# Kernel tuning notes

Hardware: AMD Instinct MI355X
Metric: run time of the kernel (lower is better)

## Reference

```python
import jax, jax.numpy as jnp
import numpy as np

B, N, P = 8, 4096, 1024
P4 = P // 4
EPS = 1e-5


def _ln(x, g, b):
    mu = jnp.mean(x, axis=-1, keepdims=True)
    var = jnp.var(x, axis=-1, keepdims=True)
    return (x - mu) * jax.lax.rsqrt(var + EPS) * g + b


def setup_inputs() -> dict:
    key = jax.random.key(0)
    ks = jax.random.split(key, 16)
    s = lambda fan: 1.0 / np.sqrt(fan)
    return {
        "xyz": jax.random.normal(ks[0], (B, N, 3), jnp.float32),
        "x": jax.random.normal(ks[1], (B, N, P), jnp.float32),
        "ln1_g": jnp.ones((P,), jnp.float32),
        "ln1_b": jnp.zeros((P,), jnp.float32),
        "ln2_g": jnp.ones((P,), jnp.float32),
        "ln2_b": jnp.zeros((P,), jnp.float32),
        "qk_w": jax.random.normal(ks[2], (P4, P), jnp.float32) * s(P),   # shared q/k 1x1 conv, no bias
        "v_w": jax.random.normal(ks[3], (P, P), jnp.float32) * s(P),
        "v_b": jax.random.normal(ks[4], (P,), jnp.float32) * s(P),
        "t1_w": jax.random.normal(ks[5], (P, P4), jnp.float32) * s(P4),  # trans_conv
        "t1_b": jax.random.normal(ks[6], (P,), jnp.float32) * s(P4),
        "t2_w": jax.random.normal(ks[7], (P, P4), jnp.float32) * s(P4),  # trans_conv1
        "t2_b": jax.random.normal(ks[8], (P,), jnp.float32) * s(P4),
        "m1_w": jax.random.normal(ks[9], (P, P), jnp.float32) * s(P),
        "m1_b": jax.random.normal(ks[10], (P,), jnp.float32) * s(P),
        "m2_w": jax.random.normal(ks[11], (P, P), jnp.float32) * s(P),
        "m2_b": jax.random.normal(ks[12], (P,), jnp.float32) * s(P),
    }


def reference(xyz, x, ln1_g, ln1_b, ln2_g, ln2_b, qk_w, v_w, v_b,
              t1_w, t1_b, t2_w, t2_b, m1_w, m1_b, m2_w, m2_b):
    # xyz is accepted but unused, matching the torch module. Dropout = eval identity.
    res1 = x
    h = _ln(x, ln1_g, ln1_b)                                   # [B,N,P]
    # TransformerBlock_1 (1x1 convs on h^T [B,P,N] are just matmuls over P)
    x_q = jnp.einsum('op,bnp->bon', qk_w, h)                   # [B,P4,N]
    # k shares weights with q; x_k permuted is x_q transposed
    x_v = jnp.einsum('op,bnp->bno', v_w, h) + v_b              # [B,N,P]
    energy = jnp.einsum('bqn,bkn->bqk', x_q, x_q)              # [B,P4,P4]
    att = jnp.einsum('op,bpk->bok', t1_w, energy) + t1_b[:, None]   # [B,P,P4]
    att = jax.nn.gelu(att, approximate=False)
    att = jnp.einsum('op,bkp->bok', t2_w, att) + t2_b[:, None]      # [B,P,P]
    att = jax.nn.softmax(att, axis=-1)
    t_out = jnp.einsum('bnp,bpq->bnq', x_v, att)               # [B,N,P]
    x1 = t_out + res1
    h2 = _ln(x1, ln2_g, ln2_b)
    m = jax.nn.gelu(h2 @ m1_w.T + m1_b, approximate=False)
    m = m @ m2_w.T + m2_b
    return x1 + m
```

## Files before the change

kernel.cpp:

```cpp
#include <hip/hip_runtime.h>


typedef __attribute__((ext_vector_type(4))) float f32x4;
typedef __attribute__((ext_vector_type(8))) _Float16 h16x8;
typedef __attribute__((ext_vector_type(8))) unsigned short u16x8;
typedef __attribute__((ext_vector_type(4))) unsigned short u16x4;

__device__ __forceinline__ unsigned short f2h(float f) {
  _Float16 h = (_Float16)f;
  return __builtin_bit_cast(unsigned short, h);
}
__device__ __forceinline__ float h2f(unsigned short u) {
  return (float)__builtin_bit_cast(_Float16, u);
}
__device__ __forceinline__ unsigned split16(float f) {
  _Float16 h = (_Float16)f;
  _Float16 l = (_Float16)(f - (float)h);
  return (unsigned)__builtin_bit_cast(unsigned short, h) |
         ((unsigned)__builtin_bit_cast(unsigned short, l) << 16);
}
__device__ __forceinline__ float gelu_f(float x) {
  return 0.5f * x * (1.0f + erff(x * 0.70710678118654752f));
}
__device__ __forceinline__ void gload16(const void* g, void* l) {
  __builtin_amdgcn_global_load_lds(
      (const __attribute__((address_space(1))) unsigned int*)g,
      (__attribute__((address_space(3))) unsigned int*)l, 16, 0, 0);
}
#define FENCE() asm volatile("" ::: "memory")

__device__ __forceinline__ void xcd_swz(int& bx, int& by, int gx, int gy) {
  const int nwg = gx * gy;
  if ((nwg & 7) == 0 && nwg >= 16) {
    const int flat = bx + gx * by;
    const int chunk = nwg >> 3;
    const int nf = (flat & 7) * chunk + (flat >> 3);
    bx = nf % gx;
    by = nf / gx;
  }
}

__global__ __launch_bounds__(256)
void ln_kernel(const float* __restrict__ x, const float* __restrict__ g,
               const float* __restrict__ b, unsigned short* __restrict__ hi,
               unsigned short* __restrict__ lo, unsigned short* __restrict__ xh) {
  __shared__ float red[16];
  const size_t base = (size_t)blockIdx.x * 1024;
  const int t = threadIdx.x;
  f32x4 v = *(const f32x4*)&x[base + t * 4];
  float s = v[0] + v[1] + v[2] + v[3];
  float q = v[0] * v[0] + v[1] * v[1] + v[2] * v[2] + v[3] * v[3];
#pragma unroll
  for (int o = 32; o > 0; o >>= 1) { s += __shfl_down(s, o); q += __shfl_down(q, o); }
  const int w = t >> 6;
  if ((t & 63) == 0) { red[w] = s; red[8 + w] = q; }
  __syncthreads();
  s = (red[0] + red[1]) + (red[2] + red[3]);
  q = (red[8] + red[9]) + (red[10] + red[11]);
  const float mu = s * (1.0f / 1024.0f);
  const float var = q * (1.0f / 1024.0f) - mu * mu;
  const float is = rsqrtf(var + 1e-5f);
  f32x4 gg = *(const f32x4*)&g[t * 4];
  f32x4 bb = *(const f32x4*)&b[t * 4];
  u16x4 oh, ol, ox;
#pragma unroll
  for (int j = 0; j < 4; j++) {
    float y = (v[j] - mu) * is * gg[j] + bb[j];
    unsigned p = split16(y);
    oh[j] = (unsigned short)(p & 0xffffu);
    ol[j] = (unsigned short)(p >> 16);
    ox[j] = f2h(v[j]);
  }
  *(u16x4*)&hi[base + t * 4] = oh;
  if (lo) *(u16x4*)&lo[base + t * 4] = ol;
  if (xh) *(u16x4*)&xh[base + t * 4] = ox;
}

__global__ __launch_bounds__(256)
void ln16_kernel(const unsigned short* __restrict__ x16, const float* __restrict__ g,
                 const float* __restrict__ b, unsigned short* __restrict__ hi) {
  __shared__ float red[16];
  const size_t base = (size_t)blockIdx.x * 1024;
  const int t = threadIdx.x;
  u16x4 raw = *(const u16x4*)&x16[base + t * 4];
  float v[4];
#pragma unroll
  for (int j = 0; j < 4; j++) v[j] = h2f(raw[j]);
  float s = v[0] + v[1] + v[2] + v[3];
  float q = v[0] * v[0] + v[1] * v[1] + v[2] * v[2] + v[3] * v[3];
#pragma unroll
  for (int o = 32; o > 0; o >>= 1) { s += __shfl_down(s, o); q += __shfl_down(q, o); }
  const int w = t >> 6;
  if ((t & 63) == 0) { red[w] = s; red[8 + w] = q; }
  __syncthreads();
  s = (red[0] + red[1]) + (red[2] + red[3]);
  q = (red[8] + red[9]) + (red[10] + red[11]);
  const float mu = s * (1.0f / 1024.0f);
  const float var = q * (1.0f / 1024.0f) - mu * mu;
  const float is = rsqrtf(var + 1e-5f);
  f32x4 gg = *(const f32x4*)&g[t * 4];
  f32x4 bb = *(const f32x4*)&b[t * 4];
  u16x4 oh;
#pragma unroll
  for (int j = 0; j < 4; j++) oh[j] = f2h((v[j] - mu) * is * gg[j] + bb[j]);
  *(u16x4*)&hi[base + t * 4] = oh;
}

__global__ __launch_bounds__(256)
void cvt_kernel(const float* __restrict__ in, unsigned short* __restrict__ hi,
                unsigned short* __restrict__ lo, int n4) {
  int i = blockIdx.x * 256 + threadIdx.x;
  if (i < n4) {
    f32x4 v = *(const f32x4*)&in[(size_t)i * 4];
    u16x4 oh, ol;
#pragma unroll
    for (int j = 0; j < 4; j++) {
      unsigned p = split16(v[j]);
      oh[j] = (unsigned short)(p & 0xffffu);
      ol[j] = (unsigned short)(p >> 16);
    }
    *(u16x4*)&hi[(size_t)i * 4] = oh;
    if (lo) *(u16x4*)&lo[(size_t)i * 4] = ol;
  }
}

__global__ __launch_bounds__(256)
void vwt_kernel(const float* __restrict__ vw, unsigned short* __restrict__ wvt) {
  __shared__ float T[64][65];
  const int bx = blockIdx.x, by = blockIdx.y;
  const int t = threadIdx.x;
  const int lr = t >> 6, lc = t & 63;
#pragma unroll
  for (int i = 0; i < 16; ++i) {
    const int row = i * 4 + lr;
    T[row][lc] = vw[(size_t)(by * 64 + row) * 1024 + bx * 64 + lc];
  }
  __syncthreads();
#pragma unroll
  for (int i = 0; i < 16; ++i) {
    const int row = i * 4 + lr;
    wvt[(size_t)(bx * 64 + row) * 1024 + by * 64 + lc] = f2h(T[lc][row]);
  }
}

__global__ __launch_bounds__(256)
void beff_kernel(const unsigned short* __restrict__ attT, const float* __restrict__ vb,
                 float* __restrict__ beff) {
  const int b = blockIdx.y;
  const int q = blockIdx.x * 4 + (threadIdx.x >> 6);
  const int l = threadIdx.x & 63;
  const unsigned short* row = attT + ((size_t)b * 1024 + q) * 1024;
  float s = 0.0f;
#pragma unroll
  for (int i = 0; i < 2; ++i) {
    u16x8 v = *(const u16x8*)&row[(i * 64 + l) * 8];
    f32x4 vb0 = *(const f32x4*)&vb[(i * 64 + l) * 8];
    f32x4 vb1 = *(const f32x4*)&vb[(i * 64 + l) * 8 + 4];
#pragma unroll
    for (int j = 0; j < 4; j++) s += h2f(v[j]) * vb0[j];
#pragma unroll
    for (int j = 0; j < 4; j++) s += h2f(v[j + 4]) * vb1[j];
  }
#pragma unroll
  for (int o = 32; o > 0; o >>= 1) s += __shfl_down(s, o);
  if (l == 0) beff[b * 1024 + q] = s;
}

template <int EPI>
__global__ __launch_bounds__(256)
void gemm_v(const unsigned short* __restrict__ Ain, const unsigned short* __restrict__ Bin,
            void* __restrict__ Cout, const float* __restrict__ bias,
            const unsigned short* __restrict__ res16In,
            int K, int lda, int ldb, int ldc,
            long long sA, long long sB, long long sC, long long sBias, long long sRes) {
  __shared__ short As[2][4096];
  __shared__ short Bs[2][4096];
  const int z = blockIdx.z;
  const unsigned short* A = Ain + (size_t)z * sA;
  const unsigned short* B = Bin + (size_t)z * sB;
  int bx = blockIdx.x, by = blockIdx.y;
  xcd_swz(bx, by, gridDim.x, gridDim.y);
  const int mBase = by * 128, nBase = bx * 128;
  const int t = threadIdx.x, w = t >> 6, l = t & 63;
  const int r16 = l & 15, kq = l >> 4;
  const int wr = (w >> 1) * 64, wc = (w & 1) * 64;
  f32x4 acc[4][4] = {};

  auto stage = [&](int buf, int k0) {
#pragma unroll
    for (int i = 0; i < 2; ++i) {
      const int c = i * 256 + t;
      const int row = c >> 2, cc = c & 3;
      const int gc = cc ^ ((row >> 1) & 3);
      short* la = &As[buf][(i * 256 + w * 64) * 8];
      short* lb = &Bs[buf][(i * 256 + w * 64) * 8];
      gload16(&A[(size_t)(mBase + row) * lda + k0 + gc * 8], la);
      gload16(&B[(size_t)(nBase + row) * ldb + k0 + gc * 8], lb);
    }
  };

  const int nt = K >> 5;
  stage(0, 0);
  if (nt > 1) stage(1, 32);
  for (int ts = 0; ts < nt; ++ts) {
    const int cur = ts & 1;
    if (ts + 1 < nt) { asm volatile("s_waitcnt vmcnt(4)" ::: "memory"); }
    else             { asm volatile("s_waitcnt vmcnt(0)" ::: "memory"); }
    __builtin_amdgcn_s_barrier();
    FENCE();
    h16x8 aF[4], bF[4];
#pragma unroll
    for (int mi = 0; mi < 4; mi++) {
      const int r = wr + mi * 16 + r16;
      aF[mi] = *(const h16x8*)&As[cur][r * 32 + (kq ^ ((r >> 1) & 3)) * 8];
    }
#pragma unroll
    for (int ni = 0; ni < 4; ni++) {
      const int r = wc + ni * 16 + r16;
      bF[ni] = *(const h16x8*)&Bs[cur][r * 32 + (kq ^ ((r >> 1) & 3)) * 8];
    }
    __builtin_amdgcn_s_setprio(1);
#pragma unroll
    for (int mi = 0; mi < 4; mi++)
#pragma unroll
      for (int ni = 0; ni < 4; ni++)
        acc[mi][ni] = __builtin_amdgcn_mfma_f32_16x16x32_f16(aF[mi], bF[ni], acc[mi][ni], 0, 0, 0);
    __builtin_amdgcn_s_setprio(0);
    FENCE();
    __builtin_amdgcn_s_barrier();
    FENCE();
    if (ts + 2 < nt) stage(cur, (ts + 2) * 32);
  }
  FENCE();

  unsigned short* C16 = (unsigned short*)Cout + (size_t)z * sC;
  float* C32 = (float*)Cout + (size_t)z * sC;
  const float* bp = (EPI == 1 || EPI == 3 || EPI == 8) ? bias + (size_t)z * sBias : nullptr;
  const unsigned short* rp = (EPI == 3 || EPI == 8) ? res16In + (size_t)z * sRes : nullptr;

  if constexpr (EPI == 1 || EPI == 4 || EPI == 8) {
    short* ep = ((w & 2) ? &Bs[0][0] : &As[0][0]) + (w & 1) * 4096;
#pragma unroll
    for (int mi = 0; mi < 4; mi++) {
#pragma unroll
      for (int ni = 0; ni < 4; ni++) {
        const int cl = nBase + wc + ni * 16 + r16;
        const float bcol = bp ? bp[cl] : 0.0f;
#pragma unroll
        for (int r = 0; r < 4; r++) {
          float v = acc[mi][ni][r] + bcol;
          if (EPI == 1) v = gelu_f(v);
          ep[(mi * 16 + kq * 4 + r) * 64 + ni * 16 + r16] = (short)f2h(v);
        }
      }
    }
#pragma unroll
    for (int j = 0; j < 8; j++) {
      const int f = j * 512 + l * 8;
      const int row = f >> 6, col = f & 63;
      u16x8 v8 = *(const u16x8*)&ep[f];
      const size_t gi = (size_t)(mBase + wr + row) * ldc + nBase + wc + col;
      if (EPI == 8) {
        u16x8 r8 = *(const u16x8*)&rp[gi];
#pragma unroll
        for (int q = 0; q < 8; q++) v8[q] = f2h(h2f(v8[q]) + h2f(r8[q]));
      }
      *(u16x8*)&C16[gi] = v8;
    }
  } else {
#pragma unroll
    for (int mi = 0; mi < 4; mi++) {
#pragma unroll
      for (int ni = 0; ni < 4; ni++) {
        const int cl = nBase + wc + ni * 16 + r16;
        const float bcol = bp[cl];
#pragma unroll
        for (int r = 0; r < 4; r++) {
          const int rw = mBase + wr + mi * 16 + kq * 4 + r;
          const size_t idx = (size_t)rw * ldc + cl;
          C32[idx] = acc[mi][ni][r] + bcol + h2f(rp[idx]);
        }
      }
    }
  }
}

template <int EPI>
__global__ __launch_bounds__(256)
void gemm_s(const unsigned short* __restrict__ Ahi, const unsigned short* __restrict__ Alo,
            const unsigned short* __restrict__ Bhi, const unsigned short* __restrict__ Blo,
            void* __restrict__ Cout, unsigned short* __restrict__ Cout2,
            const float* __restrict__ bias,
            int K, int lda, int ldb, int ldc,
            long long sA, long long sB, long long sC, int splitK) {
  __shared__ short As[2][8192];
  __shared__ short Bs[2][8192];
  const int z = blockIdx.z;
  const int bi = z / splitK, sp = z % splitK;
  const int kLen = K / splitK, kStart = sp * kLen;
  const unsigned short* AH = Ahi + (size_t)bi * sA;
  const unsigned short* BH = Bhi + (size_t)bi * sB;
  const unsigned short* AL = Alo + (size_t)bi * sA;
  const unsigned short* BL = Blo + (size_t)bi * sB;
  int bx = blockIdx.x, by = blockIdx.y;
  xcd_swz(bx, by, gridDim.x, gridDim.y);
  const int mBase = by * 128, nBase = bx * 128;
  const int t = threadIdx.x, w = t >> 6, l = t & 63;
  const int r16 = l & 15, kq = l >> 4;
  const int wr = (w >> 1) * 64, wc = (w & 1) * 64;
  f32x4 acc[4][4] = {};

  auto stage = [&](int buf, int k0) {
#pragma unroll
    for (int i = 0; i < 2; ++i) {
      const int c = i * 256 + t;
      const int row = c >> 2, cc = c & 3;
      const int gc = cc ^ ((row >> 1) & 3);
      const int cbase = i * 256 + w * 64;
      const size_t ga = (size_t)(mBase + row) * lda + k0 + gc * 8;
      const size_t gb = (size_t)(nBase + row) * ldb + k0 + gc * 8;
      gload16(&AH[ga], &As[buf][cbase * 8]);
      gload16(&AL[ga], &As[buf][4096 + cbase * 8]);
      gload16(&BH[gb], &Bs[buf][cbase * 8]);
      gload16(&BL[gb], &Bs[buf][4096 + cbase * 8]);
    }
  };

  const int nsteps = kLen >> 5;
  stage(0, kStart);
  if (nsteps > 1) stage(1, kStart + 32);
  for (int ts = 0; ts < nsteps; ++ts) {
    const int cur = ts & 1;
    if (ts + 1 < nsteps) { asm volatile("s_waitcnt vmcnt(8)" ::: "memory"); }
    else                 { asm volatile("s_waitcnt vmcnt(0)" ::: "memory"); }
    __builtin_amdgcn_s_barrier();
    FENCE();
    h16x8 aH[4], bH[4], aL[4], bL[4];
#pragma unroll
    for (int mi = 0; mi < 4; mi++) {
      const int r = wr + mi * 16 + r16;
      const int off = r * 32 + (kq ^ ((r >> 1) & 3)) * 8;
      aH[mi] = *(const h16x8*)&As[cur][off];
      aL[mi] = *(const h16x8*)&As[cur][4096 + off];
    }
#pragma unroll
    for (int ni = 0; ni < 4; ni++) {
      const int r = wc + ni * 16 + r16;
      const int off = r * 32 + (kq ^ ((r >> 1) & 3)) * 8;
      bH[ni] = *(const h16x8*)&Bs[cur][off];
      bL[ni] = *(const h16x8*)&Bs[cur][4096 + off];
    }
    __builtin_amdgcn_s_setprio(1);
#pragma unroll
    for (int mi = 0; mi < 4; mi++)
#pragma unroll
      for (int ni = 0; ni < 4; ni++) {
        acc[mi][ni] = __builtin_amdgcn_mfma_f32_16x16x32_f16(aH[mi], bH[ni], acc[mi][ni], 0, 0, 0);
        acc[mi][ni] = __builtin_amdgcn_mfma_f32_16x16x32_f16(aH[mi], bL[ni], acc[mi][ni], 0, 0, 0);
        acc[mi][ni] = __builtin_amdgcn_mfma_f32_16x16x32_f16(aL[mi], bH[ni], acc[mi][ni], 0, 0, 0);
      }
    __builtin_amdgcn_s_setprio(0);
    FENCE();
    __builtin_amdgcn_s_barrier();
    FENCE();
    if (ts + 2 < nsteps) stage(cur, kStart + (ts + 2) * 32);
  }
  FENCE();

  unsigned short* C16 = (unsigned short*)Cout + (size_t)z * sC;
  unsigned short* C16b = Cout2 ? Cout2 + (size_t)z * sC : nullptr;
  float* C32 = (float*)Cout + (size_t)z * sC;

  if constexpr (EPI == 4 || EPI == 6) {
    short* ep = &As[0][0] + w * 4096;
    unsigned pk[4][4][4];
#pragma unroll
    for (int mi = 0; mi < 4; mi++)
#pragma unroll
      for (int ni = 0; ni < 4; ni++)
#pragma unroll
        for (int r = 0; r < 4; r++) {
          float v = acc[mi][ni][r];
          if (EPI == 6) { v += bias[mBase + wr + mi * 16 + kq * 4 + r]; v = gelu_f(v); }
          pk[mi][ni][r] = split16(v);
        }
#pragma unroll
    for (int mi = 0; mi < 4; mi++)
#pragma unroll
      for (int ni = 0; ni < 4; ni++)
#pragma unroll
        for (int r = 0; r < 4; r++)
          ep[(mi * 16 + kq * 4 + r) * 64 + ni * 16 + r16] =
              (short)(pk[mi][ni][r] & 0xffffu);
#pragma unroll
    for (int j = 0; j < 8; j++) {
      const int f = j * 512 + l * 8;
      const int row = f >> 6, col = f & 63;
      *(u16x8*)&C16[(size_t)(mBase + wr + row) * ldc + nBase + wc + col] =
          *(const u16x8*)&ep[f];
    }
#pragma unroll
    for (int mi = 0; mi < 4; mi++)
#pragma unroll
      for (int ni = 0; ni < 4; ni++)
#pragma unroll
        for (int r = 0; r < 4; r++)
          ep[(mi * 16 + kq * 4 + r) * 64 + ni * 16 + r16] =
              (short)(pk[mi][ni][r] >> 16);
#pragma unroll
    for (int j = 0; j < 8; j++) {
      const int f = j * 512 + l * 8;
      const int row = f >> 6, col = f & 63;
      *(u16x8*)&C16b[(size_t)(mBase + wr + row) * ldc + nBase + wc + col] =
          *(const u16x8*)&ep[f];
    }
  } else {
#pragma unroll
    for (int mi = 0; mi < 4; mi++) {
#pragma unroll
      for (int ni = 0; ni < 4; ni++) {
        const int cl = nBase + wc + ni * 16 + r16;
#pragma unroll
        for (int r = 0; r < 4; r++) {
          const int rw = mBase + wr + mi * 16 + kq * 4 + r;
          float v = acc[mi][ni][r];
          if (EPI == 7) v += bias[rw];
          C32[(size_t)rw * ldc + cl] = v;
        }
      }
    }
  }
}

__global__ __launch_bounds__(256)
void ereduce_kernel(const float* __restrict__ part, unsigned short* __restrict__ ehi,
                    unsigned short* __restrict__ elo) {
  const size_t idx = (size_t)blockIdx.x * 256 + threadIdx.x;
  const size_t b = idx >> 16, i = idx & 65535;
  const float* p = part + b * (8ull * 65536) + i;
  float s0 = (p[0] + p[65536]) + (p[2 * 65536] + p[3 * 65536]);
  float s1 = (p[4 * 65536] + p[5 * 65536]) + (p[6 * 65536] + p[7 * 65536]);
  unsigned pk = split16(s0 + s1);
  ehi[idx] = (unsigned short)(pk & 0xffffu);
  elo[idx] = (unsigned short)(pk >> 16);
}

__global__ __launch_bounds__(256)
void smax_t_kernel(const float* __restrict__ a2, unsigned short* __restrict__ attT) {
  __shared__ float S[8][1028];
  __shared__ float inv[8];
  const int t = threadIdx.x;
  const int b = blockIdx.y;
  const int o0 = blockIdx.x * 8;
  const float* src = a2 + ((size_t)b * 1024 + o0) * 1024;
#pragma unroll
  for (int i = 0; i < 8; i++)
    *(f32x4*)&S[i][t * 4] = *(const f32x4*)&src[(size_t)i * 1024 + t * 4];
  __syncthreads();
  const int w = t >> 6, l = t & 63;
  for (int rr = 0; rr < 2; rr++) {
    const int r = w * 2 + rr;
    float m = -1e30f;
#pragma unroll
    for (int i = 0; i < 16; i++) m = fmaxf(m, S[r][l + i * 64]);
#pragma unroll
    for (int o = 32; o > 0; o >>= 1) m = fmaxf(m, __shfl_xor(m, o));
    float ssum = 0.0f;
#pragma unroll
    for (int i = 0; i < 16; i++) {
      float e = expf(S[r][l + i * 64] - m);
      S[r][l + i * 64] = e;
      ssum += e;
    }
#pragma unroll
    for (int o = 32; o > 0; o >>= 1) ssum += __shfl_xor(ssum, o);
    if (l == 0) inv[r] = 1.0f / ssum;
  }
  __syncthreads();
  float iv[8];
#pragma unroll
  for (int r = 0; r < 8; r++) iv[r] = inv[r];
#pragma unroll
  for (int i = 0; i < 4; i++) {
    const int k = i * 256 + t;
    u16x8 ov;
#pragma unroll
    for (int r = 0; r < 8; r++) ov[r] = f2h(S[r][k] * iv[r]);
    *(u16x8*)&attT[((size_t)b * 1024 + k) * 1024 + o0] = ov;
  }
}

extern "C" void kernel_launch(void* const* d_in, const int* in_sizes, int n_in,
                              void* d_out, int out_size, void* d_ws, size_t ws_size,
                              hipStream_t stream) {
  (void)in_sizes; (void)n_in; (void)out_size; (void)ws_size;
  const float* x     = (const float*)d_in[1];
  const float* ln1_g = (const float*)d_in[2];
  const float* ln1_b = (const float*)d_in[3];
  const float* ln2_g = (const float*)d_in[4];
  const float* ln2_b = (const float*)d_in[5];
  const float* qk_w  = (const float*)d_in[6];
  const float* v_w   = (const float*)d_in[7];
  const float* v_b   = (const float*)d_in[8];
  const float* t1_w  = (const float*)d_in[9];
  const float* t1_b  = (const float*)d_in[10];
  const float* t2_w  = (const float*)d_in[11];
  const float* t2_b  = (const float*)d_in[12];
  const float* m1_w  = (const float*)d_in[13];
  const float* m1_b  = (const float*)d_in[14];
  const float* m2_w  = (const float*)d_in[15];
  const float* m2_b  = (const float*)d_in[16];

  char* ws = (char*)d_ws;
  unsigned short* hhi  = (unsigned short*)(ws + 0);
  unsigned short* hlo  = (unsigned short*)(ws + 67108864);
  unsigned short* Qthi = (unsigned short*)(ws + 134217728);
  unsigned short* Qtlo = (unsigned short*)(ws + 150994944);
  float*          part = (float*)(ws + 167772160);
  unsigned short* Ehi  = (unsigned short*)(ws + 184549376);
  unsigned short* Elo  = (unsigned short*)(ws + 185597952);
  unsigned short* Ghi  = (unsigned short*)(ws + 186646528);
  unsigned short* Glo  = (unsigned short*)(ws + 190840832);
  float*          a2   = (float*)(ws + 195035136);
  unsigned short* attT = (unsigned short*)(ws + 228589568);
  unsigned short* WeT  = (unsigned short*)(ws + 245366784);
  float*          beff = (float*)(ws + 262144000);
  unsigned short* xh   = (unsigned short*)(ws + 268435456);
  unsigned short* x1h  = (unsigned short*)(ws + 335544320);
  unsigned short* wqh  = (unsigned short*)(ws + 446693376);
  unsigned short* wql  = (unsigned short*)(ws + 447217664);
  unsigned short* wvt  = (unsigned short*)(ws + 447741952);
  unsigned short* wt1h = (unsigned short*)(ws + 449839104);
  unsigned short* wt1l = (unsigned short*)(ws + 450363392);
  unsigned short* wt2h = (unsigned short*)(ws + 450887680);
  unsigned short* wt2l = (unsigned short*)(ws + 451411968);
  unsigned short* wm1  = (unsigned short*)(ws + 451936256);
  unsigned short* wm2  = (unsigned short*)(ws + 454033408);
  unsigned short* h2 = hhi;
  unsigned short* gb = hlo;
  float* out = (float*)d_out;

  cvt_kernel<<<dim3(256),  dim3(256), 0, stream>>>(qk_w, wqh, wql, 65536);
  vwt_kernel<<<dim3(16, 16), dim3(256), 0, stream>>>(v_w, wvt);
  cvt_kernel<<<dim3(256),  dim3(256), 0, stream>>>(t1_w, wt1h, wt1l, 65536);
  cvt_kernel<<<dim3(256),  dim3(256), 0, stream>>>(t2_w, wt2h, wt2l, 65536);
  cvt_kernel<<<dim3(1024), dim3(256), 0, stream>>>(m1_w, wm1, nullptr, 262144);
  cvt_kernel<<<dim3(1024), dim3(256), 0, stream>>>(m2_w, wm2, nullptr, 262144);
  ln_kernel<<<dim3(32768), dim3(256), 0, stream>>>(x, ln1_g, ln1_b, hhi, hlo, xh);
  gemm_s<4><<<dim3(32, 2, 8), dim3(256), 0, stream>>>(
      wqh, wql, hhi, hlo, Qthi, Qtlo, nullptr,
      1024, 1024, 1024, 4096, 0, 4194304, 1048576, 1);
  gemm_s<5><<<dim3(2, 2, 64), dim3(256), 0, stream>>>(
      Qthi, Qtlo, Qthi, Qtlo, part, nullptr, nullptr,
      4096, 4096, 4096, 256, 1048576, 1048576, 65536, 8);
  ereduce_kernel<<<dim3(2048), dim3(256), 0, stream>>>(part, Ehi, Elo);
  gemm_s<6><<<dim3(2, 8, 8), dim3(256), 0, stream>>>(
      wt1h, wt1l, Ehi, Elo, Ghi, Glo, t1_b,
      256, 256, 256, 256, 0, 65536, 262144, 1);
  gemm_s<7><<<dim3(8, 8, 8), dim3(256), 0, stream>>>(
      wt2h, wt2l, Ghi, Glo, a2, nullptr, t2_b,
      256, 256, 256, 1024, 0, 262144, 1048576, 1);
  smax_t_kernel<<<dim3(128, 8), dim3(256), 0, stream>>>(a2, attT);
  gemm_v<4><<<dim3(8, 8, 8), dim3(256), 0, stream>>>(
      attT, wvt, WeT, nullptr, nullptr,
      1024, 1024, 1024, 1024, 1048576, 0, 1048576, 0, 0);
  beff_kernel<<<dim3(256, 8), dim3(256), 0, stream>>>(attT, v_b, beff);
  gemm_v<8><<<dim3(8, 32, 8), dim3(256), 0, stream>>>(
      hhi, WeT, x1h, beff, xh,
      1024, 1024, 1024, 1024, 4194304, 1048576, 4194304, 1024, 4194304);
  ln16_kernel<<<dim3(32768), dim3(256), 0, stream>>>(x1h, ln2_g, ln2_b, h2);
  gemm_v<1><<<dim3(8, 256, 1), dim3(256), 0, stream>>>(
      h2, wm1, gb, m1_b, nullptr, 1024, 1024, 1024, 1024, 0, 0, 0, 0, 0);
  gemm_v<3><<<dim3(8, 256, 1), dim3(256), 0, stream>>>(
      gb, wm2, out, m2_b, x1h, 1024, 1024, 1024, 1024, 0, 0, 0, 0, 0);
}
```

Measured before the change: 655.0 us.

## Fuse LN2 normalization into MLP1 GEMM load path and stage epilogues via LDS

```diff
diff --git a/kernel.cpp b/kernel.cpp
--- a/kernel.cpp
+++ b/kernel.cpp
@@ -77,8 +77,7 @@
 }
 
 __global__ __launch_bounds__(256)
-void ln16_kernel(const unsigned short* __restrict__ x16, const float* __restrict__ g,
-                 const float* __restrict__ b, unsigned short* __restrict__ hi) {
+void stats16_kernel(const unsigned short* __restrict__ x16, float* __restrict__ muis) {
   __shared__ float red[16];
   const size_t base = (size_t)blockIdx.x * 1024;
   const int t = threadIdx.x;
@@ -93,17 +92,14 @@
   const int w = t >> 6;
   if ((t & 63) == 0) { red[w] = s; red[8 + w] = q; }
   __syncthreads();
-  s = (red[0] + red[1]) + (red[2] + red[3]);
-  q = (red[8] + red[9]) + (red[10] + red[11]);
-  const float mu = s * (1.0f / 1024.0f);
-  const float var = q * (1.0f / 1024.0f) - mu * mu;
-  const float is = rsqrtf(var + 1e-5f);
-  f32x4 gg = *(const f32x4*)&g[t * 4];
-  f32x4 bb = *(const f32x4*)&b[t * 4];
-  u16x4 oh;
-#pragma unroll
-  for (int j = 0; j < 4; j++) oh[j] = f2h((v[j] - mu) * is * gg[j] + bb[j]);
-  *(u16x4*)&hi[base + t * 4] = oh;
+  if (t == 0) {
+    s = (red[0] + red[1]) + (red[2] + red[3]);
+    q = (red[8] + red[9]) + (red[10] + red[11]);
+    const float mu = s * (1.0f / 1024.0f);
+    const float var = q * (1.0f / 1024.0f) - mu * mu;
+    muis[blockIdx.x * 2] = mu;
+    muis[blockIdx.x * 2 + 1] = rsqrtf(var + 1e-5f);
+  }
 }
 
 __global__ __launch_bounds__(256)
@@ -285,7 +281,234 @@
   }
 }
 
-template <int EPI>
+__global__ __launch_bounds__(256)
+void gemm_r(const unsigned short* __restrict__ Ain, const unsigned short* __restrict__ Bin,
+            unsigned short* __restrict__ Cout, const float* __restrict__ bias,
+            const unsigned short* __restrict__ resIn,
+            int K, int lda, int ldb, int ldc,
+            long long sA, long long sB, long long sC, long long sBias, long long sRes) {
+  __shared__ short As[2][4096];
+  __shared__ short Bs[2][4096];
+  const int z = blockIdx.z;
+  const unsigned short* A = Ain + (size_t)z * sA;
+  const unsigned short* B = Bin + (size_t)z * sB;
+  int bx = blockIdx.x, by = blockIdx.y;
+  xcd_swz(bx, by, gridDim.x, gridDim.y);
+  const int mBase = by * 128, nBase = bx * 128;
+  const int t = threadIdx.x, w = t >> 6, l = t & 63;
+  const int r16 = l & 15, kq = l >> 4;
+  const int wr = (w >> 1) * 64, wc = (w & 1) * 64;
+  f32x4 acc[4][4] = {};
+
+  const int row0 = t >> 2, row1 = 64 + (t >> 2);
+  const int cc0 = t & 3;
+  const int gc0 = cc0 ^ ((row0 >> 1) & 3);
+  const int gc1 = cc0 ^ ((row1 >> 1) & 3);
+
+  u16x8 ra0, ra1, rb0, rb1;
+  auto loadreg = [&](int k0) {
+    ra0 = *(const u16x8*)&A[(size_t)(mBase + row0) * lda + k0 + gc0 * 8];
+    rb0 = *(const u16x8*)&B[(size_t)(nBase + row0) * ldb + k0 + gc0 * 8];
+    ra1 = *(const u16x8*)&A[(size_t)(mBase + row1) * lda + k0 + gc1 * 8];
+    rb1 = *(const u16x8*)&B[(size_t)(nBase + row1) * ldb + k0 + gc1 * 8];
+  };
+  auto dswrite = [&](int buf) {
+    *(u16x8*)&As[buf][t * 8] = ra0;
+    *(u16x8*)&Bs[buf][t * 8] = rb0;
+    *(u16x8*)&As[buf][(256 + t) * 8] = ra1;
+    *(u16x8*)&Bs[buf][(256 + t) * 8] = rb1;
+  };
+
+  const int nt = K >> 5;
+  loadreg(0);
+  dswrite(0);
+  if (nt > 1) loadreg(32);
+  asm volatile("s_waitcnt lgkmcnt(0)" ::: "memory");
+  __builtin_amdgcn_s_barrier();
+  FENCE();
+  for (int ts = 0; ts < nt; ++ts) {
+    const int cur = ts & 1;
+    h16x8 aF[4], bF[4];
+#pragma unroll
+    for (int mi = 0; mi < 4; mi++) {
+      const int r = wr + mi * 16 + r16;
+      aF[mi] = *(const h16x8*)&As[cur][r * 32 + (kq ^ ((r >> 1) & 3)) * 8];
+    }
+#pragma unroll
+    for (int ni = 0; ni < 4; ni++) {
+      const int r = wc + ni * 16 + r16;
+      bF[ni] = *(const h16x8*)&Bs[cur][r * 32 + (kq ^ ((r >> 1) & 3)) * 8];
+    }
+    __builtin_amdgcn_s_setprio(1);
+#pragma unroll
+    for (int mi = 0; mi < 4; mi++)
+#pragma unroll
+      for (int ni = 0; ni < 4; ni++)
+        acc[mi][ni] = __builtin_amdgcn_mfma_f32_16x16x32_f16(aF[mi], bF[ni], acc[mi][ni], 0, 0, 0);
+    __builtin_amdgcn_s_setprio(0);
+    FENCE();
+    if (ts + 1 < nt) {
+      __builtin_amdgcn_s_barrier();
+      FENCE();
+      dswrite((ts + 1) & 1);
+      if (ts + 2 < nt) loadreg((ts + 2) * 32);
+      asm volatile("s_waitcnt lgkmcnt(0)" ::: "memory");
+      FENCE();
+      __builtin_amdgcn_s_barrier();
+      FENCE();
+    }
+  }
+  FENCE();
+
+  unsigned short* C16 = Cout + (size_t)z * sC;
+  const float* bp = bias + (size_t)z * sBias;
+  const unsigned short* rp = resIn + (size_t)z * sRes;
+  short* ep = ((w & 2) ? &Bs[0][0] : &As[0][0]) + (w & 1) * 4096;
+#pragma unroll
+  for (int mi = 0; mi < 4; mi++) {
+#pragma unroll
+    for (int ni = 0; ni < 4; ni++) {
+      const int cl = nBase + wc + ni * 16 + r16;
+      const float bcol = bp[cl];
+#pragma unroll
+      for (int r = 0; r < 4; r++)
+        ep[(mi * 16 + kq * 4 + r) * 64 + ni * 16 + r16] =
+            (short)f2h(acc[mi][ni][r] + bcol);
+    }
+  }
+#pragma unroll
+  for (int j = 0; j < 8; j++) {
+    const int f = j * 512 + l * 8;
+    const int row = f >> 6, col = f & 63;
+    u16x8 v8 = *(const u16x8*)&ep[f];
+    const size_t gi = (size_t)(mBase + wr + row) * ldc + nBase + wc + col;
+    u16x8 r8 = *(const u16x8*)&rp[gi];
+#pragma unroll
+    for (int q = 0; q < 8; q++) v8[q] = f2h(h2f(v8[q]) + h2f(r8[q]));
+    *(u16x8*)&C16[gi] = v8;
+  }
+}
+
+__global__ __launch_bounds__(256)
+void gemm_m(const unsigned short* __restrict__ Ain, const unsigned short* __restrict__ Bin,
+            const float* __restrict__ muis, const float* __restrict__ lng,
+            const float* __restrict__ lnb, const float* __restrict__ bias,
+            unsigned short* __restrict__ Cout, int K, int lda, int ldb, int ldc) {
+  __shared__ short As[2][4096];
+  __shared__ short Bs[2][4096];
+  int bx = blockIdx.x, by = blockIdx.y;
+  xcd_swz(bx, by, gridDim.x, gridDim.y);
+  const int mBase = by * 128, nBase = bx * 128;
+  const int t = threadIdx.x, w = t >> 6, l = t & 63;
+  const int r16 = l & 15, kq = l >> 4;
+  const int wr = (w >> 1) * 64, wc = (w & 1) * 64;
+  f32x4 acc[4][4] = {};
+
+  const int row0 = t >> 2, row1 = 64 + (t >> 2);
+  const int cc0 = t & 3;
+  const int gc0 = cc0 ^ ((row0 >> 1) & 3);
+  const int gc1 = cc0 ^ ((row1 >> 1) & 3);
+  const float mu0 = muis[(mBase + row0) * 2], is0 = muis[(mBase + row0) * 2 + 1];
+  const float mu1 = muis[(mBase + row1) * 2], is1 = muis[(mBase + row1) * 2 + 1];
+
+  u16x8 ra0, ra1, rb0, rb1;
+  auto loadreg = [&](int k0) {
+    ra0 = *(const u16x8*)&Ain[(size_t)(mBase + row0) * lda + k0 + gc0 * 8];
+    rb0 = *(const u16x8*)&Bin[(size_t)(nBase + row0) * ldb + k0 + gc0 * 8];
+    ra1 = *(const u16x8*)&Ain[(size_t)(mBase + row1) * lda + k0 + gc1 * 8];
+    rb1 = *(const u16x8*)&Bin[(size_t)(nBase + row1) * ldb + k0 + gc1 * 8];
+  };
+  auto dswrite = [&](int buf, int k0) {
+    {
+      const int cb = k0 + gc0 * 8;
+      f32x4 g0 = *(const f32x4*)&lng[cb], g1 = *(const f32x4*)&lng[cb + 4];
+      f32x4 b0 = *(const f32x4*)&lnb[cb], b1 = *(const f32x4*)&lnb[cb + 4];
+      u16x8 o;
+#pragma unroll
+      for (int j = 0; j < 4; j++) o[j] = f2h((h2f(ra0[j]) - mu0) * is0 * g0[j] + b0[j]);
+#pragma unroll
+      for (int j = 0; j < 4; j++) o[j + 4] = f2h((h2f(ra0[j + 4]) - mu0) * is0 * g1[j] + b1[j]);
+      *(u16x8*)&As[buf][t * 8] = o;
+      *(u16x8*)&Bs[buf][t * 8] = rb0;
+    }
+    {
+      const int cb = k0 + gc1 * 8;
+      f32x4 g0 = *(const f32x4*)&lng[cb], g1 = *(const f32x4*)&lng[cb + 4];
+      f32x4 b0 = *(const f32x4*)&lnb[cb], b1 = *(const f32x4*)&lnb[cb + 4];
+      u16x8 o;
+#pragma unroll
+      for (int j = 0; j < 4; j++) o[j] = f2h((h2f(ra1[j]) - mu1) * is1 * g0[j] + b0[j]);
+#pragma unroll
+      for (int j = 0; j < 4; j++) o[j + 4] = f2h((h2f(ra1[j + 4]) - mu1) * is1 * g1[j] + b1[j]);
+      *(u16x8*)&As[buf][(256 + t) * 8] = o;
+      *(u16x8*)&Bs[buf][(256 + t) * 8] = rb1;
+    }
+  };
+
+  const int nt = K >> 5;
+  loadreg(0);
+  dswrite(0, 0);
+  if (nt > 1) loadreg(32);
+  asm volatile("s_waitcnt lgkmcnt(0)" ::: "memory");
+  __builtin_amdgcn_s_barrier();
+  FENCE();
+  for (int ts = 0; ts < nt; ++ts) {
+    const int cur = ts & 1;
+    h16x8 aF[4], bF[4];
+#pragma unroll
+    for (int mi = 0; mi < 4; mi++) {
+      const int r = wr + mi * 16 + r16;
+      aF[mi] = *(const h16x8*)&As[cur][r * 32 + (kq ^ ((r >> 1) & 3)) * 8];
+    }
+#pragma unroll
+    for (int ni = 0; ni < 4; ni++) {
+      const int r = wc + ni * 16 + r16;
+      bF[ni] = *(const h16x8*)&Bs[cur][r * 32 + (kq ^ ((r >> 1) & 3)) * 8];
+    }
+    __builtin_amdgcn_s_setprio(1);
+#pragma unroll
+    for (int mi = 0; mi < 4; mi++)
+#pragma unroll
+      for (int ni = 0; ni < 4; ni++)
+        acc[mi][ni] = __builtin_amdgcn_mfma_f32_16x16x32_f16(aF[mi], bF[ni], acc[mi][ni], 0, 0, 0);
+    __builtin_amdgcn_s_setprio(0);
+    FENCE();
+    if (ts + 1 < nt) {
+      __builtin_amdgcn_s_barrier();
+      FENCE();
+      dswrite((ts + 1) & 1, (ts + 1) * 32);
+      if (ts + 2 < nt) loadreg((ts + 2) * 32);
+      asm volatile("s_waitcnt lgkmcnt(0)" ::: "memory");
+      FENCE();
+      __builtin_amdgcn_s_barrier();
+      FENCE();
+    }
+  }
+  FENCE();
+
+  short* ep = ((w & 2) ? &Bs[0][0] : &As[0][0]) + (w & 1) * 4096;
+#pragma unroll
+  for (int mi = 0; mi < 4; mi++) {
+#pragma unroll
+    for (int ni = 0; ni < 4; ni++) {
+      const int cl = nBase + wc + ni * 16 + r16;
+      const float bcol = bias[cl];
+#pragma unroll
+      for (int r = 0; r < 4; r++)
+        ep[(mi * 16 + kq * 4 + r) * 64 + ni * 16 + r16] =
+            (short)f2h(gelu_f(acc[mi][ni][r] + bcol));
+    }
+  }
+#pragma unroll
+  for (int j = 0; j < 8; j++) {
+    const int f = j * 512 + l * 8;
+    const int row = f >> 6, col = f & 63;
+    *(u16x8*)&Cout[(size_t)(mBase + wr + row) * ldc + nBase + wc + col] =
+        *(const u16x8*)&ep[f];
+  }
+}
+
+template <int EPI, int SWAP>
 __global__ __launch_bounds__(256)
 void gemm_s(const unsigned short* __restrict__ Ahi, const unsigned short* __restrict__ Alo,
             const unsigned short* __restrict__ Bhi, const unsigned short* __restrict__ Blo,
@@ -304,7 +527,7 @@
   const unsigned short* BL = Blo + (size_t)bi * sB;
   int bx = blockIdx.x, by = blockIdx.y;
   xcd_swz(bx, by, gridDim.x, gridDim.y);
-  const int mBase = by * 128, nBase = bx * 128;
+  const int mBase = (SWAP ? bx : by) * 128, nBase = (SWAP ? by : bx) * 128;
   const int t = threadIdx.x, w = t >> 6, l = t & 63;
   const int r16 = l & 15, kq = l >> 4;
   const int wr = (w >> 1) * 64, wc = (w & 1) * 64;
@@ -525,6 +748,7 @@
   unsigned short* attT = (unsigned short*)(ws + 228589568);
   unsigned short* WeT  = (unsigned short*)(ws + 245366784);
   float*          beff = (float*)(ws + 262144000);
+  float*          muis = (float*)(ws + 262176768);
   unsigned short* xh   = (unsigned short*)(ws + 268435456);
   unsigned short* x1h  = (unsigned short*)(ws + 335544320);
   unsigned short* wqh  = (unsigned short*)(ws + 446693376);
@@ -536,7 +760,6 @@
   unsigned short* wt2l = (unsigned short*)(ws + 451411968);
   unsigned short* wm1  = (unsigned short*)(ws + 451936256);
   unsigned short* wm2  = (unsigned short*)(ws + 454033408);
-  unsigned short* h2 = hhi;
   unsigned short* gb = hlo;
   float* out = (float*)d_out;
 
@@ -547,17 +770,17 @@
   cvt_kernel<<<dim3(1024), dim3(256), 0, stream>>>(m1_w, wm1, nullptr, 262144);
   cvt_kernel<<<dim3(1024), dim3(256), 0, stream>>>(m2_w, wm2, nullptr, 262144);
   ln_kernel<<<dim3(32768), dim3(256), 0, stream>>>(x, ln1_g, ln1_b, hhi, hlo, xh);
-  gemm_s<4><<<dim3(32, 2, 8), dim3(256), 0, stream>>>(
+  gemm_s<4, 1><<<dim3(2, 32, 8), dim3(256), 0, stream>>>(
       wqh, wql, hhi, hlo, Qthi, Qtlo, nullptr,
       1024, 1024, 1024, 4096, 0, 4194304, 1048576, 1);
-  gemm_s<5><<<dim3(2, 2, 64), dim3(256), 0, stream>>>(
+  gemm_s<5, 0><<<dim3(2, 2, 64), dim3(256), 0, stream>>>(
       Qthi, Qtlo, Qthi, Qtlo, part, nullptr, nullptr,
       4096, 4096, 4096, 256, 1048576, 1048576, 65536, 8);
   ereduce_kernel<<<dim3(2048), dim3(256), 0, stream>>>(part, Ehi, Elo);
-  gemm_s<6><<<dim3(2, 8, 8), dim3(256), 0, stream>>>(
+  gemm_s<6, 0><<<dim3(2, 8, 8), dim3(256), 0, stream>>>(
       wt1h, wt1l, Ehi, Elo, Ghi, Glo, t1_b,
       256, 256, 256, 256, 0, 65536, 262144, 1);
-  gemm_s<7><<<dim3(8, 8, 8), dim3(256), 0, stream>>>(
+  gemm_s<7, 0><<<dim3(8, 8, 8), dim3(256), 0, stream>>>(
       wt2h, wt2l, Ghi, Glo, a2, nullptr, t2_b,
       256, 256, 256, 1024, 0, 262144, 1048576, 1);
   smax_t_kernel<<<dim3(128, 8), dim3(256), 0, stream>>>(a2, attT);
@@ -565,12 +788,12 @@
       attT, wvt, WeT, nullptr, nullptr,
       1024, 1024, 1024, 1024, 1048576, 0, 1048576, 0, 0);
   beff_kernel<<<dim3(256, 8), dim3(256), 0, stream>>>(attT, v_b, beff);
-  gemm_v<8><<<dim3(8, 32, 8), dim3(256), 0, stream>>>(
+  gemm_r<<<dim3(8, 32, 8), dim3(256), 0, stream>>>(
       hhi, WeT, x1h, beff, xh,
       1024, 1024, 1024, 1024, 4194304, 1048576, 4194304, 1024, 4194304);
-  ln16_kernel<<<dim3(32768), dim3(256), 0, stream>>>(x1h, ln2_g, ln2_b, h2);
-  gemm_v<1><<<dim3(8, 256, 1), dim3(256), 0, stream>>>(
-      h2, wm1, gb, m1_b, nullptr, 1024, 1024, 1024, 1024, 0, 0, 0, 0, 0);
+  stats16_kernel<<<dim3(32768), dim3(256), 0, stream>>>(x1h, muis);
+  gemm_m<<<dim3(8, 256, 1), dim3(256), 0, stream>>>(
+      x1h, wm1, muis, ln2_g, ln2_b, m1_b, gb, 1024, 1024, 1024, 1024);
   gemm_v<3><<<dim3(8, 256, 1), dim3(256), 0, stream>>>(
       gb, wm2, out, m2_b, x1h, 1024, 1024, 1024, 1024, 0, 0, 0, 0, 0);
 }
```

After: 660.9 us. No clear change (+0.9%).
